# Kernel optimization log

Hardware: AMD Instinct MI355X
Metric: run time of the kernel (lower is better)

Reference implementation:

```python
import jax, jax.numpy as jnp
import numpy as np
import math

EPS = 1e-20
TEMP = 0.07


def _affinity(x1, x2, n):
    # x1, x2: (B, C, T-1, N+1); use only the first n (non-dustbin) nodes
    A = jnp.einsum('bctn,bctm->btnm', x1[..., :n], x2[..., :n])  # (B,T-1,n,n)
    # entropy of row-normalized affinities (intended math of Categorical(probs=A[b,t,k]).entropy())
    p = A / A.sum(-1, keepdims=True)
    ent = -(p * jnp.log(jnp.maximum(p, EPS))).sum(-1)            # (B,T-1,n)
    dustbin_w = 1.0 / math.log(n)
    A = jnp.concatenate([A, (ent * dustbin_w)[..., None]], axis=-1)  # (B,T-1,n,n+1)
    dust_row = -A.sum(-2)[:, :, None, :]                              # (B,T-1,1,n+1)
    A = jnp.concatenate([A, dust_row], axis=2)                        # (B,T-1,n+1,n+1)
    A = A.at[:, :, -1, -1].set(0.0)
    return A


def _l2norm(x, axis):
    return x / jnp.maximum(jnp.linalg.norm(x, axis=axis, keepdims=True), 1e-12)


def _forward(feats_raw, dust_raw, W_self, b_self, W_dust, b_dust):
    B, N, Cenc, T = feats_raw.shape
    # selfsim head: Linear over channel dim, then L2-normalize features
    f = jnp.einsum('bnct,cd->bndt', feats_raw, W_self) + b_self[None, None, :, None]
    f = _l2norm(f, axis=2)                      # (B,N,128,T)
    q = jnp.transpose(f, (0, 2, 3, 1))          # (B,128,T,N)
    d = jnp.einsum('bct,cd->bdt', dust_raw, W_dust) + b_dust[None, :, None]
    d = _l2norm(d, axis=1)                      # (B,128,T)
    q = jnp.concatenate([q, d[..., None]], axis=-1)  # (B,128,T,N+1)

    Af = _affinity(q[:, :, :-1], q[:, :, 1:], N)
    qf = jnp.flip(q, axis=2)
    Ab = _affinity(qf[:, :, :-1], qf[:, :, 1:], N)

    A12 = jax.nn.softmax(Af / TEMP, axis=-1)    # (B,T-1,M,M)
    A21 = jax.nn.softmax(Ab / TEMP, axis=-1)

    M = N + 1
    tgt = jnp.tile(jnp.arange(M), B)            # (B*M,)
    rows = jnp.arange(B * M)
    left = A12[:, 0]
    right = A21[:, T - 2]
    losses = []
    for i in range(1, T - 1):                   # fixed small loop over time steps
        left = left @ A12[:, i]
        right = A21[:, T - 2 - i] @ right
        AA = left @ right                       # (B,M,M) palindrome walk
        logits = jnp.log(AA + EPS).reshape(-1, M)
        ls = jax.nn.log_softmax(logits, axis=-1)
        losses.append(-ls[rows, tgt].mean())
    loss = sum(losses) / len(losses)
    return q, loss


def setup_inputs() -> dict:
    key = jax.random.key(0)
    ks = jax.random.split(key, 4)
    B, N, C, T, D = 4, 784, 512, 8, 128
    return {
        'feats_raw': jax.random.normal(ks[0], (B, N, C, T), dtype=jnp.float32),
        'dust_raw': jax.random.normal(ks[1], (B, C, T), dtype=jnp.float32),
        'W_self': jax.random.normal(ks[2], (C, D), dtype=jnp.float32) * 0.05,
        'b_self': jnp.zeros((D,), dtype=jnp.float32),
        'W_dust': jax.random.normal(ks[3], (C, D), dtype=jnp.float32) * 0.05,
        'b_dust': jnp.zeros((D,), dtype=jnp.float32),
    }


def reference(feats_raw, dust_raw, W_self, b_self, W_dust, b_dust):
    return _forward(feats_raw, dust_raw, W_self, b_self, W_dust, b_dust)
```

## Files before the change

### kernel.cpp

```cpp
#include <hip/hip_runtime.h>
#include <hip/hip_bf16.h>
#include <math.h>

constexpr int Bc = 4;
constexpr int Nc = 784;
constexpr int Cc = 512;
constexpr int Tc = 8;
constexpr int Dc = 128;
constexpr int Mc = 785;
constexpr int TM1 = 7;
constexpr int Pp = 832;
constexpr int Qrows = 896;
constexpr float TEMP = 0.07f;

typedef __attribute__((ext_vector_type(4))) float f32x4;
typedef __attribute__((ext_vector_type(8))) unsigned short u16x8;
typedef __attribute__((ext_vector_type(8))) __bf16 bf16x8;

__device__ __forceinline__ unsigned short f2bf(float v) {
    __hip_bfloat16 h = __float2bfloat16(v);
    return __builtin_bit_cast(unsigned short, h);
}
__device__ __forceinline__ float bf2f(unsigned short u) {
    return __builtin_bit_cast(float, (unsigned int)u << 16);
}

__device__ __forceinline__ void gload16(const void* g, void* l) {
    __builtin_amdgcn_global_load_lds(
        (const __attribute__((address_space(1))) unsigned int*)g,
        (__attribute__((address_space(3))) unsigned int*)l, 16, 0, 0);
}

template<int LD>
__device__ __forceinline__ void mfma_tile_loop(const unsigned short* __restrict__ A,
                                               const unsigned short* __restrict__ BT,
                                               unsigned short* __restrict__ As,
                                               unsigned short* __restrict__ Bs,
                                               int i0, int j0, int tid,
                                               f32x4 (&acc)[4][4])
{
    const int lane = tid & 63, w = tid >> 6;
    const int wr = w >> 1, wc = w & 1;
    const int g = lane >> 4, lr = lane & 15;

    for (int k0 = 0; k0 < LD; k0 += 64) {
        __syncthreads();
        #pragma unroll
        for (int q = 0; q < 4; ++q) {
            int L16 = q * 256 + tid;
            int r = L16 >> 3;
            int csw = ((L16 & 7) << 4) ^ ((r & 7) << 4);
            const char* ga = (const char*)(A  + (size_t)(i0 + r) * LD + k0) + csw;
            const char* gb = (const char*)(BT + (size_t)(j0 + r) * LD + k0) + csw;
            gload16(ga, As + (size_t)L16 * 8);
            gload16(gb, Bs + (size_t)L16 * 8);
        }
        __syncthreads();
        #pragma unroll
        for (int ks = 0; ks < 2; ++ks) {
            bf16x8 af[4], bf[4];
            #pragma unroll
            for (int m = 0; m < 4; ++m) {
                int r = wr * 64 + m * 16 + lr;
                int cb = (ks * 64 + g * 16) ^ ((r & 7) << 4);
                af[m] = __builtin_bit_cast(bf16x8, *(const u16x8*)((const char*)As + r * 128 + cb));
            }
            #pragma unroll
            for (int n = 0; n < 4; ++n) {
                int r = wc * 64 + n * 16 + lr;
                int cb = (ks * 64 + g * 16) ^ ((r & 7) << 4);
                bf[n] = __builtin_bit_cast(bf16x8, *(const u16x8*)((const char*)Bs + r * 128 + cb));
            }
            #pragma unroll
            for (int m = 0; m < 4; ++m)
                #pragma unroll
                for (int n = 0; n < 4; ++n)
                    acc[m][n] = __builtin_amdgcn_mfma_f32_16x16x32_bf16(af[m], bf[n], acc[m][n], 0, 0, 0);
        }
    }
}

__device__ __forceinline__ float blockReduceSum(float v, float* sbuf) {
    #pragma unroll
    for (int off = 32; off; off >>= 1) v += __shfl_down(v, off, 64);
    __syncthreads();
    if ((threadIdx.x & 63) == 0) sbuf[threadIdx.x >> 6] = v;
    __syncthreads();
    return sbuf[0] + sbuf[1] + sbuf[2] + sbuf[3];
}
__device__ __forceinline__ float blockReduceMax(float v, float* sbuf) {
    #pragma unroll
    for (int off = 32; off; off >>= 1) v = fmaxf(v, __shfl_down(v, off, 64));
    __syncthreads();
    if ((threadIdx.x & 63) == 0) sbuf[threadIdx.x >> 6] = v;
    __syncthreads();
    return fmaxf(fmaxf(sbuf[0], sbuf[1]), fmaxf(sbuf[2], sbuf[3]));
}

__global__ __launch_bounds__(256) void k_pack(const float* __restrict__ feats,
                                              unsigned int* __restrict__ Abf32)
{
    __shared__ float lds[Cc * 9];
    int bid = blockIdx.x;
    int b = bid / Nc, n = bid % Nc;
    const float* src = feats + (size_t)(b * Nc + n) * Cc * Tc;
    int tid = threadIdx.x;
    for (int i = tid; i < Cc * Tc; i += 256) lds[(i >> 3) * 9 + (i & 7)] = src[i];
    __syncthreads();
    #pragma unroll
    for (int t = 0; t < Tc; ++t) {
        size_t row = (size_t)(b * Tc + t) * Nc + n;
        float v0 = lds[(2 * tid) * 9 + t];
        float v1 = lds[(2 * tid + 1) * 9 + t];
        unsigned int pk = (unsigned int)f2bf(v0) | ((unsigned int)f2bf(v1) << 16);
        Abf32[row * (Cc / 2) + tid] = pk;
    }
}

__global__ __launch_bounds__(256) void k_packw(const float* __restrict__ Wself,
                                               const float* __restrict__ Wdust,
                                               unsigned short* __restrict__ WTb)
{
    __shared__ float tile[64][65];
    int which = blockIdx.z;
    const float* W = which ? Wdust : Wself;
    unsigned short* O = WTb + (size_t)which * Dc * Cc;
    int d0 = blockIdx.x * 64, c0 = blockIdx.y * 64;
    int tx = threadIdx.x & 63, ty = threadIdx.x >> 6;
    #pragma unroll
    for (int y = 0; y < 64; y += 4) tile[y + ty][tx] = W[(size_t)(c0 + y + ty) * Dc + d0 + tx];
    __syncthreads();
    #pragma unroll
    for (int y = 0; y < 64; y += 4) O[(size_t)(d0 + y + ty) * Cc + c0 + tx] = f2bf(tile[tx][y + ty]);
}

__global__ __launch_bounds__(256, 3) void k_gemm_proj(const unsigned short* __restrict__ A,
                                                      const unsigned short* __restrict__ BT,
                                                      const float* __restrict__ bias,
                                                      float* __restrict__ Cf)
{
    __shared__ __align__(16) unsigned short As[128 * 64];
    __shared__ __align__(16) unsigned short Bs[128 * 64];
    const int i0 = blockIdx.y * 128;
    const int tid = threadIdx.x, lane = tid & 63, w = tid >> 6;
    const int wr = w >> 1, wc = w & 1;
    const int g = lane >> 4, lr = lane & 15;

    f32x4 acc[4][4] = {};
    mfma_tile_loop<Cc>(A, BT, As, Bs, i0, 0, tid, acc);

    #pragma unroll
    for (int n = 0; n < 4; ++n) {
        int col = wc * 64 + n * 16 + lr;
        float bv = bias[col];
        #pragma unroll
        for (int m = 0; m < 4; ++m)
            #pragma unroll
            for (int j = 0; j < 4; ++j) {
                int row = i0 + wr * 64 + m * 16 + g * 4 + j;
                Cf[(size_t)row * Dc + col] = acc[m][n][j] + bv;
            }
    }
}

__global__ __launch_bounds__(128) void k_dustproj(const float* __restrict__ dust,
                                                  const float* __restrict__ Wdust,
                                                  const float* __restrict__ bdust,
                                                  unsigned short* __restrict__ qTb,
                                                  float* __restrict__ qout)
{
    __shared__ float sdust[Cc];
    __shared__ float red[2];
    int bt = blockIdx.x;
    int b = bt >> 3, t = bt & 7;
    int tid = threadIdx.x;
    for (int i = tid; i < Cc; i += 128) sdust[i] = dust[((size_t)b * Cc + i) * Tc + t];
    __syncthreads();
    float acc = 0.f;
    for (int c = 0; c < Cc; ++c) acc += sdust[c] * Wdust[(size_t)c * Dc + tid];
    acc += bdust[tid];
    float s = acc * acc;
    #pragma unroll
    for (int off = 32; off; off >>= 1) s += __shfl_down(s, off, 64);
    if ((tid & 63) == 0) red[tid >> 6] = s;
    __syncthreads();
    float inv = 1.f / fmaxf(sqrtf(red[0] + red[1]), 1e-12f);
    float qv = acc * inv;
    qTb[((size_t)bt * Qrows + Nc) * Dc + tid] = f2bf(qv);
    qout[(((size_t)b * Dc + tid) * Tc + t) * Mc + Nc] = qv;
}

__global__ __launch_bounds__(256) void k_norm(const float* __restrict__ fbuf,
                                              unsigned short* __restrict__ qTb,
                                              float* __restrict__ qout)
{
    __shared__ float lds[64][129];
    __shared__ float nrm[64][4];
    __shared__ float inv[64];
    int bt = blockIdx.y;
    int b = bt >> 3, t = bt & 7;
    int n0 = blockIdx.x * 64;
    int tid = threadIdx.x;
    #pragma unroll
    for (int q = 0; q < 8; ++q) {
        int i = q * 256 + tid;
        int nl = i >> 5, d4 = i & 31;
        f32x4 v = {};
        if (n0 + nl < Nc) v = *(const f32x4*)(fbuf + ((size_t)bt * Nc + n0 + nl) * Dc + d4 * 4);
        *(f32x4*)(&lds[nl][d4 * 4]) = v;
    }
    __syncthreads();
    {
        int r = tid & 63, p = tid >> 6;
        float s = 0.f;
        #pragma unroll
        for (int j = 0; j < 32; ++j) { float v = lds[r][p * 32 + j]; s += v * v; }
        nrm[r][p] = s;
    }
    __syncthreads();
    if (tid < 64) inv[tid] = 1.f / fmaxf(sqrtf(nrm[tid][0] + nrm[tid][1] + nrm[tid][2] + nrm[tid][3]), 1e-12f);
    __syncthreads();
    unsigned int* qT32 = (unsigned int*)(qTb + (size_t)bt * Qrows * Dc);
    #pragma unroll
    for (int q = 0; q < 16; ++q) {
        int i = q * 256 + tid;
        int nl = i >> 6, dp = i & 63;
        if (n0 + nl < Nc) {
            float iv = inv[nl];
            unsigned int pk = (unsigned int)f2bf(lds[nl][2 * dp] * iv)
                            | ((unsigned int)f2bf(lds[nl][2 * dp + 1] * iv) << 16);
            qT32[((size_t)(n0 + nl) * Dc >> 1) + dp] = pk;
        }
    }
    int nl = tid & 63;
    if (n0 + nl < Nc) {
        float iv = inv[nl];
        #pragma unroll
        for (int dd = 0; dd < Dc; dd += 4) {
            int d = dd + (tid >> 6);
            qout[(((size_t)b * Dc + d) * Tc + t) * Mc + n0 + nl] = lds[nl][d] * iv;
        }
    }
}

__global__ __launch_bounds__(256) void k_affinity(const unsigned short* __restrict__ qTb,
                                                  unsigned short* __restrict__ P12h,
                                                  unsigned short* __restrict__ P21h,
                                                  float* __restrict__ cs12,
                                                  float* __restrict__ cs21,
                                                  float wconst)
{
    constexpr float INVT = 1.0f / TEMP;
    const size_t MMp = (size_t)Pp * Pp;
    __shared__ unsigned short otile[16][840];
    __shared__ float sred[16][4][2];
    __shared__ float rowsum[16], invZ[16], entP[16];

    int f = blockIdx.x;
    int xcd = f & 7, slot = f >> 3;
    int grp = xcd + 8 * (slot / 49);
    int strip = slot % 49;
    int side = grp >= 28 ? 1 : 0;
    int bt = grp - side * 28;
    int b = bt / TM1, t = bt % TM1;
    const unsigned short *Aq, *Bq;
    unsigned short* OUT;
    if (side == 0) {
        Aq = qTb + (size_t)(b * Tc + t)     * Qrows * Dc;
        Bq = qTb + (size_t)(b * Tc + t + 1) * Qrows * Dc;
        OUT = P12h + (size_t)bt * MMp;
    } else {
        Aq = qTb + (size_t)(b * Tc + 7 - t) * Qrows * Dc;
        Bq = qTb + (size_t)(b * Tc + 6 - t) * Qrows * Dc;
        OUT = P21h + (size_t)bt * MMp;
    }
    float* csFlip = (side == 0 ? cs21 : cs12) + (size_t)(b * TM1 + (6 - t)) * Pp;

    const int r0 = strip * 16;
    const int tid = threadIdx.x, lane = tid & 63, w = tid >> 6;
    const int g = lane >> 4, lr = lane & 15;

    f32x4 acc[13] = {};
    #pragma unroll
    for (int ks = 0; ks < 4; ++ks) {
        bf16x8 af = __builtin_bit_cast(bf16x8,
            *(const u16x8*)(Aq + (size_t)(r0 + lr) * Dc + ks * 32 + g * 8));
        bf16x8 bfr[7];
        #pragma unroll
        for (int tt = 0; tt < 7; ++tt)
            if (w * 13 + tt < 49)
                bfr[tt] = __builtin_bit_cast(bf16x8,
                    *(const u16x8*)(Bq + (size_t)((w * 13 + tt) * 16 + lr) * Dc + ks * 32 + g * 8));
        #pragma unroll
        for (int tt = 0; tt < 7; ++tt)
            if (w * 13 + tt < 49)
                acc[tt] = __builtin_amdgcn_mfma_f32_16x16x32_bf16(af, bfr[tt], acc[tt], 0, 0, 0);
        #pragma unroll
        for (int tt = 7; tt < 13; ++tt)
            if (w * 13 + tt < 49)
                bfr[tt - 7] = __builtin_bit_cast(bf16x8,
                    *(const u16x8*)(Bq + (size_t)((w * 13 + tt) * 16 + lr) * Dc + ks * 32 + g * 8));
        #pragma unroll
        for (int tt = 7; tt < 13; ++tt)
            if (w * 13 + tt < 49)
                acc[tt] = __builtin_amdgcn_mfma_f32_16x16x32_bf16(af, bfr[tt - 7], acc[tt], 0, 0, 0);
    }

    float rs[4] = {0.f, 0.f, 0.f, 0.f};
    #pragma unroll
    for (int tt = 0; tt < 13; ++tt) {
        if (w * 13 + tt < 49) {
            #pragma unroll
            for (int j = 0; j < 4; ++j) rs[j] += acc[tt][j];
        }
    }
    #pragma unroll
    for (int off = 1; off <= 8; off <<= 1) {
        #pragma unroll
        for (int j = 0; j < 4; ++j) rs[j] += __shfl_xor(rs[j], off, 64);
    }
    if (lr == 0) {
        #pragma unroll
        for (int j = 0; j < 4; ++j) sred[g * 4 + j][w][0] = rs[j];
    }
    __syncthreads();
    if (tid < 16) {
        float r = sred[tid][0][0] + sred[tid][1][0] + sred[tid][2][0] + sred[tid][3][0];
        rowsum[tid] = r;
        csFlip[r0 + tid] = r;
    }
    __syncthreads();

    float invr[4];
    #pragma unroll
    for (int j = 0; j < 4; ++j) invr[j] = 1.0f / rowsum[g * 4 + j];
    float en[4] = {0.f, 0.f, 0.f, 0.f}, es[4] = {0.f, 0.f, 0.f, 0.f};
    #pragma unroll
    for (int tt = 0; tt < 13; ++tt) {
        if (w * 13 + tt < 49) {
            #pragma unroll
            for (int j = 0; j < 4; ++j) {
                float a = acc[tt][j];
                float e = __expf(a * INVT);
                es[j] += e;
                float p = a * invr[j];
                en[j] -= p * __logf(fmaxf(p, 1e-20f));
                acc[tt][j] = e;
            }
        }
    }
    #pragma unroll
    for (int off = 1; off <= 8; off <<= 1) {
        #pragma unroll
        for (int j = 0; j < 4; ++j) {
            es[j] += __shfl_xor(es[j], off, 64);
            en[j] += __shfl_xor(en[j], off, 64);
        }
    }
    if (lr == 0) {
        #pragma unroll
        for (int j = 0; j < 4; ++j) { sred[g * 4 + j][w][0] = es[j]; sred[g * 4 + j][w][1] = en[j]; }
    }
    __syncthreads();
    if (tid < 16) {
        float esum = sred[tid][0][0] + sred[tid][1][0] + sred[tid][2][0] + sred[tid][3][0];
        float ent  = sred[tid][0][1] + sred[tid][1][1] + sred[tid][2][1] + sred[tid][3][1];
        float ez  = __expf(ent * wconst * INVT);
        float Z   = esum + ez;
        float iz  = 1.0f / Z;
        invZ[tid] = iz;
        entP[tid] = ez * iz;
    }
    __syncthreads();

    float izl[4];
    #pragma unroll
    for (int j = 0; j < 4; ++j) izl[j] = invZ[g * 4 + j];
    #pragma unroll
    for (int tt = 0; tt < 13; ++tt) {
        int gt = w * 13 + tt;
        if (gt < 49) {
            int col = gt * 16 + lr;
            #pragma unroll
            for (int j = 0; j < 4; ++j)
                otile[g * 4 + j][col] = f2bf(acc[tt][j] * izl[j]);
        }
    }
    if (tid < 16) otile[tid][784] = f2bf(entP[tid]);
    for (int i = tid; i < 16 * 47; i += 256) otile[i / 47][785 + i % 47] = 0;
    __syncthreads();

    for (int v = tid; v < 16 * 104; v += 256) {
        int row = v / 104, cv = v % 104;
        *(u16x8*)(OUT + (size_t)(r0 + row) * Pp + cv * 8) = *(const u16x8*)(&otile[row][cv * 8]);
    }
}

__global__ __launch_bounds__(256) void k_dustrow(const float* __restrict__ cs12,
                                                 const float* __restrict__ cs21,
                                                 unsigned short* __restrict__ P12h,
                                                 unsigned short* __restrict__ P21h)
{
    constexpr float INVT = 1.0f / TEMP;
    const size_t MMp = (size_t)Pp * Pp;
    int bt = blockIdx.x, side = blockIdx.y;
    const float* cs = (side ? cs21 : cs12) + (size_t)bt * Pp;
    unsigned short* OUT = (side ? P21h : P12h) + (size_t)bt * MMp;
    __shared__ float sbuf[4];
    int tid = threadIdx.x;
    float v[4];
    #pragma unroll
    for (int k = 0; k < 4; ++k) {
        int j = tid + k * 256;
        float val = -INFINITY;
        if (j < Nc)       val = -cs[j] * INVT;
        else if (j == Nc) val = 0.f;
        v[k] = val;
    }
    float mx = fmaxf(fmaxf(v[0], v[1]), fmaxf(v[2], v[3]));
    mx = blockReduceMax(mx, sbuf);
    float e[4]; float s = 0.f;
    #pragma unroll
    for (int k = 0; k < 4; ++k) {
        int j = tid + k * 256;
        e[k] = (j < Mc) ? __expf(v[k] - mx) : 0.f;
        s += e[k];
    }
    s = blockReduceSum(s, sbuf);
    float invs = 1.f / s;
    #pragma unroll
    for (int k = 0; k < 4; ++k) {
        int j = tid + k * 256;
        if (j < Mc)      OUT[(size_t)Nc * Pp + j] = f2bf(e[k] * invs);
        else if (j < Pp) OUT[(size_t)Nc * Pp + j] = 0;
    }
    u16x8 z = {};
    u16x8* dst = (u16x8*)(OUT + (size_t)785 * Pp);
    for (int i = tid; i < (Pp - 785) * Pp / 8; i += 256) dst[i] = z;
}

__global__ __launch_bounds__(256) void k_transpose_bf16(const unsigned short* __restrict__ P12h,
                                                        const unsigned short* __restrict__ P21h,
                                                        unsigned short* __restrict__ Db)
{
    const size_t MMp = (size_t)Pp * Pp;
    __shared__ unsigned short tile[64][65];
    int z = blockIdx.z;
    const unsigned short* S;
    if (z < 24) { int b = z / 6, tm = z % 6; S = P12h + ((size_t)b * 7 + tm + 1) * MMp; }
    else        { S = P21h + ((size_t)(z - 24) * 7 + 6) * MMp; }
    unsigned short* D = Db + (size_t)z * MMp;
    int x0 = blockIdx.x * 64, y0 = blockIdx.y * 64;
    int tx = threadIdx.x & 63, ty = threadIdx.x >> 6;
    #pragma unroll
    for (int y = 0; y < 64; y += 4) tile[y + ty][tx] = S[(size_t)(y0 + y + ty) * Pp + x0 + tx];
    __syncthreads();
    #pragma unroll
    for (int y = 0; y < 64; y += 4) D[(size_t)(x0 + y + ty) * Pp + y0 + tx] = tile[tx][y + ty];
}

struct GJobs {
    const unsigned short* A[2];
    const unsigned short* BT[2];
    unsigned short* Cb[2];
    float* cs[2];
    long long sA[2], sB[2], sC[2];
    const unsigned short* Lr;
    const unsigned short* Rr;
    const float* csL;
    float* loss;
    float scale;
};

__global__ __launch_bounds__(256, 4) void k_gemm_loss(GJobs J)
{
    const size_t MMp = (size_t)Pp * Pp;
    if (blockIdx.x >= 728) {
        int q = blockIdx.x - 728;
        int w = threadIdx.x >> 6, lane = threadIdx.x & 63;
        int r = q * 4 + w;
        int b = r / Mc, i = r % Mc;
        const u16x8* lrow = (const u16x8*)(J.Lr + (size_t)b * MMp + (size_t)i * Pp);
        const u16x8* rrow = (const u16x8*)(J.Rr + (size_t)b * MMp + (size_t)i * Pp);
        const f32x4* cs4  = (const f32x4*)(J.csL + (size_t)b * Pp);
        float sR = 0.f, sD = 0.f;
        for (int c = lane; c < Pp / 8; c += 64) {
            u16x8 lv = lrow[c];
            u16x8 rv = rrow[c];
            f32x4 c0 = cs4[2 * c], c1 = cs4[2 * c + 1];
            #pragma unroll
            for (int k = 0; k < 4; ++k) {
                float fl = bf2f(lv[k]);
                sR += fl * c0[k];
                sD += fl * bf2f(rv[k]);
            }
            #pragma unroll
            for (int k = 0; k < 4; ++k) {
                float fl = bf2f(lv[4 + k]);
                sR += fl * c1[k];
                sD += fl * bf2f(rv[4 + k]);
            }
        }
        #pragma unroll
        for (int off = 1; off <= 32; off <<= 1) {
            sR += __shfl_xor(sR, off, 64);
            sD += __shfl_xor(sD, off, 64);
        }
        if (lane == 0)
            atomicAdd(J.loss, (logf(sR + Mc * 1e-20f) - logf(sD + 1e-20f)) * J.scale);
        return;
    }

    __shared__ __align__(16) unsigned short As[64 * 64];
    __shared__ __align__(16) unsigned short Bs[128 * 64];

    int f = blockIdx.x;
    int zz = f & 7, slot = f >> 3;
    int job = zz >> 2, b = zz & 3;
    const unsigned short* A  = J.A[job]  + (size_t)b * J.sA[job];
    const unsigned short* BT = J.BT[job] + (size_t)b * J.sB[job];

    const int i0 = (slot / 7) * 64, j0 = (slot % 7) * 128;
    const int tid = threadIdx.x, lane = tid & 63, wv = tid >> 6;
    const int g = lane >> 4, lr = lane & 15;

    f32x4 acc[4][2] = {};

    for (int k0 = 0; k0 < Pp; k0 += 64) {
        __syncthreads();
        #pragma unroll
        for (int q = 0; q < 2; ++q) {
            int s = q * 256 + tid;
            int r = s >> 3;
            int csw = ((s & 7) << 4) ^ ((r & 7) << 4);
            gload16((const char*)(A + (size_t)(i0 + r) * Pp + k0) + csw, As + (size_t)s * 8);
        }
        #pragma unroll
        for (int q = 0; q < 4; ++q) {
            int s = q * 256 + tid;
            int r = s >> 3;
            int csw = ((s & 7) << 4) ^ ((r & 7) << 4);
            gload16((const char*)(BT + (size_t)(j0 + r) * Pp + k0) + csw, Bs + (size_t)s * 8);
        }
        __syncthreads();
        #pragma unroll
        for (int ks = 0; ks < 2; ++ks) {
            bf16x8 af[4], bf[2];
            #pragma unroll
            for (int m = 0; m < 4; ++m) {
                int r = m * 16 + lr;
                int cb = (ks * 64 + g * 16) ^ ((r & 7) << 4);
                af[m] = __builtin_bit_cast(bf16x8, *(const u16x8*)((const char*)As + r * 128 + cb));
            }
            #pragma unroll
            for (int n = 0; n < 2; ++n) {
                int r = wv * 32 + n * 16 + lr;
                int cb = (ks * 64 + g * 16) ^ ((r & 7) << 4);
                bf[n] = __builtin_bit_cast(bf16x8, *(const u16x8*)((const char*)Bs + r * 128 + cb));
            }
            #pragma unroll
            for (int m = 0; m < 4; ++m)
                #pragma unroll
                for (int n = 0; n < 2; ++n)
                    acc[m][n] = __builtin_amdgcn_mfma_f32_16x16x32_bf16(af[m], bf[n], acc[m][n], 0, 0, 0);
        }
    }

    unsigned short* Co = J.Cb[job] + (size_t)b * J.sC[job];
    float* csp = J.cs[job];
    float csacc[2] = {0.f, 0.f};
    #pragma unroll
    for (int m = 0; m < 4; ++m)
        #pragma unroll
        for (int n = 0; n < 2; ++n)
            #pragma unroll
            for (int j = 0; j < 4; ++j) {
                int row = i0 + m * 16 + g * 4 + j;
                int col = j0 + wv * 32 + n * 16 + lr;
                if (col < Pp) {
                    unsigned short h = f2bf(acc[m][n][j]);
                    Co[(size_t)row * Pp + col] = h;
                    csacc[n] += bf2f(h);
                }
            }
    if (csp) {
        csp += (size_t)b * Pp;
        #pragma unroll
        for (int n = 0; n < 2; ++n) {
            float p = csacc[n];
            p += __shfl_xor(p, 16, 64);
            p += __shfl_xor(p, 32, 64);
            int col = j0 + wv * 32 + n * 16 + lr;
            if (g == 0 && col < Pp) atomicAdd(&csp[col], p);
        }
    }
}

__global__ __launch_bounds__(64) void k_lossrow(const unsigned short* __restrict__ L,
                                                const unsigned short* __restrict__ R,
                                                const float* __restrict__ csR,
                                                float* __restrict__ loss, float scale)
{
    const size_t MMp = (size_t)Pp * Pp;
    int r = blockIdx.x;
    int b = r / Mc, i = r % Mc;
    const u16x8* lrow = (const u16x8*)(L + (size_t)b * MMp + (size_t)i * Pp);
    const u16x8* rrow = (const u16x8*)(R + (size_t)b * MMp + (size_t)i * Pp);
    const f32x4* cs4  = (const f32x4*)(csR + (size_t)b * Pp);
    int lane = threadIdx.x;
    float sR = 0.f, sD = 0.f;
    for (int c = lane; c < Pp / 8; c += 64) {
        u16x8 lv = lrow[c];
        u16x8 rv = rrow[c];
        f32x4 c0 = cs4[2 * c], c1 = cs4[2 * c + 1];
        #pragma unroll
        for (int k = 0; k < 4; ++k) {
            float fl = bf2f(lv[k]);
            sR += fl * c0[k];
            sD += fl * bf2f(rv[k]);
        }
        #pragma unroll
        for (int k = 0; k < 4; ++k) {
            float fl = bf2f(lv[4 + k]);
            sR += fl * c1[k];
            sD += fl * bf2f(rv[4 + k]);
        }
    }
    #pragma unroll
    for (int off = 1; off <= 32; off <<= 1) {
        sR += __shfl_xor(sR, off, 64);
        sD += __shfl_xor(sD, off, 64);
    }
    if (lane == 0)
        atomicAdd(loss, (logf(sR + Mc * 1e-20f) - logf(sD + 1e-20f)) * scale);
}

extern "C" void kernel_launch(void* const* d_in, const int* in_sizes, int n_in,
                              void* d_out, int out_size, void* d_ws, size_t ws_size,
                              hipStream_t stream)
{
    const float* feats = (const float*)d_in[0];
    const float* dust  = (const float*)d_in[1];
    const float* Wself = (const float*)d_in[2];
    const float* bself = (const float*)d_in[3];
    const float* Wdust = (const float*)d_in[4];
    const float* bdust = (const float*)d_in[5];

    float* out  = (float*)d_out;
    float* qout = out;
    float* loss = out + (size_t)Bc * Dc * Tc * Mc;

    const size_t MMp = (size_t)Pp * Pp;

    float* ws = (float*)d_ws;
    float* csR = ws;
    unsigned short* P12h = (unsigned short*)(ws + 4 * MMp);
    unsigned short* P21h = P12h + (size_t)28 * MMp;
    unsigned short* chainT = P21h + (size_t)28 * MMp;
    unsigned short* P12T  = chainT;
    unsigned short* P21T6 = P12T + (size_t)24 * MMp;
    unsigned short* l0    = P21T6 + (size_t)4 * MMp;
    unsigned short* l1    = l0 + (size_t)4 * MMp;
    unsigned short* R0    = l1 + (size_t)4 * MMp;
    unsigned short* R1    = R0 + (size_t)4 * MMp;
    unsigned short* qTb   = R1 + (size_t)4 * MMp;
    float* cs12 = (float*)(qTb + (size_t)32 * Qrows * Dc);
    float* cs21 = cs12 + (size_t)28 * Pp;

    unsigned short* Abf   = chainT;
    unsigned int*   Abf32 = (unsigned int*)Abf;
    unsigned short* WTb   = Abf + (size_t)Bc * Tc * Nc * Cc;
    float*          fbuf  = (float*)(WTb + 2 * (size_t)Dc * Cc);

    k_pack<<<Bc * Nc, 256, 0, stream>>>(feats, Abf32);
    k_packw<<<dim3(2, 8, 2), 256, 0, stream>>>(Wself, Wdust, WTb);
    hipMemsetAsync(csR, 0, (size_t)6 * Bc * Pp * sizeof(float), stream);
    hipMemsetAsync(loss, 0, sizeof(float), stream);
    k_gemm_proj<<<dim3(1, 196), 256, 0, stream>>>(Abf, WTb, bself, fbuf);
    k_dustproj<<<32, 128, 0, stream>>>(dust, Wdust, bdust, qTb, qout);
    k_norm<<<dim3(13, 32), 256, 0, stream>>>(fbuf, qTb, qout);
    float wconst = (float)(1.0 / log(784.0));
    k_affinity<<<2744, 256, 0, stream>>>(qTb, P12h, P21h, cs12, cs21, wconst);
    k_dustrow<<<dim3(28, 2), 256, 0, stream>>>(cs12, cs21, P12h, P21h);
    k_transpose_bf16<<<dim3(13, 13, 28), 256, 0, stream>>>(P12h, P21h, P12T);

    const float scale = 1.0f / (6.0f * Bc * Mc);

    {
        GJobs J = {};
        J.A[0] = P12h;  J.sA[0] = (long long)7 * MMp;
        J.BT[0] = P12T; J.sB[0] = (long long)6 * MMp;
        J.Cb[0] = l0;   J.sC[0] = (long long)MMp; J.cs[0] = nullptr;
        J.A[1] = P21T6;                   J.sA[1] = (long long)MMp;
        J.BT[1] = P21h + (size_t)5 * MMp; J.sB[1] = (long long)7 * MMp;
        J.Cb[1] = R0;   J.sC[1] = (long long)MMp; J.cs[1] = csR;
        k_gemm_loss<<<728, 256, 0, stream>>>(J);
    }

    unsigned short *lcur = l0, *lnxt = l1, *rcur = R0, *rnxt = R1;
    for (int i = 1; i <= 5; ++i) {
        GJobs J = {};
        J.A[0] = lcur; J.sA[0] = (long long)MMp;
        J.BT[0] = P12T + (size_t)i * MMp; J.sB[0] = (long long)6 * MMp;
        J.Cb[0] = lnxt; J.sC[0] = (long long)MMp; J.cs[0] = nullptr;
        J.A[1] = rcur; J.sA[1] = (long long)MMp;
        J.BT[1] = P21h + (size_t)(5 - i) * MMp; J.sB[1] = (long long)7 * MMp;
        J.Cb[1] = rnxt; J.sC[1] = (long long)MMp; J.cs[1] = csR + (size_t)i * Bc * Pp;
        J.Lr = lcur; J.Rr = rcur; J.csL = csR + (size_t)(i - 1) * Bc * Pp;
        J.loss = loss; J.scale = scale;
        k_gemm_loss<<<728 + 785, 256, 0, stream>>>(J);
        unsigned short* t;
        t = lcur; lcur = lnxt; lnxt = t;
        t = rcur; rcur = rnxt; rnxt = t;
    }
    k_lossrow<<<Bc * Mc, 64, 0, stream>>>(lcur, rcur, csR + (size_t)5 * Bc * Pp, loss, scale);
}
```

Measured before the change: 481.6 us.

## Double-buffer GEMM tiles, shrink projection tiles, and fuse small setup kernels

Adds a shared double-buffered 64x128 MFMA GEMM helper that prefetches the next K-tile into a second LDS buffer while the current one is computed, and uses it in both the projection GEMM and the loss-chain GEMM. The projection GEMM moves from 128x128 tiles on 196 blocks to 64x128 tiles on 392 blocks. Weight packing, buffer zeroing and the dustbin projection are folded into existing kernels as extra blocks, which removes separate launches and memsets. Launch bounds are changed (affinity 2 waves/SIMD hint, loss GEMM from 4 to 3) to fit the doubled LDS, at the cost of lower occupancy.

```diff
diff --git a/kernel.cpp b/kernel.cpp
--- a/kernel.cpp
+++ b/kernel.cpp
@@ -32,51 +32,74 @@
 }
 
 template<int LD>
-__device__ __forceinline__ void mfma_tile_loop(const unsigned short* __restrict__ A,
-                                               const unsigned short* __restrict__ BT,
-                                               unsigned short* __restrict__ As,
-                                               unsigned short* __restrict__ Bs,
-                                               int i0, int j0, int tid,
-                                               f32x4 (&acc)[4][4])
-{
-    const int lane = tid & 63, w = tid >> 6;
-    const int wr = w >> 1, wc = w & 1;
+__device__ __forceinline__ void gemm64x128_db(const unsigned short* __restrict__ A,
+                                              const unsigned short* __restrict__ BT,
+                                              unsigned short* As0, unsigned short* As1,
+                                              unsigned short* Bs0, unsigned short* Bs1,
+                                              int i0, int j0, int tid, f32x4 (&acc)[4][2])
+{
+    const int lane = tid & 63, wv = tid >> 6;
     const int g = lane >> 4, lr = lane & 15;
-
-    for (int k0 = 0; k0 < LD; k0 += 64) {
-        __syncthreads();
-        #pragma unroll
-        for (int q = 0; q < 4; ++q) {
-            int L16 = q * 256 + tid;
-            int r = L16 >> 3;
-            int csw = ((L16 & 7) << 4) ^ ((r & 7) << 4);
-            const char* ga = (const char*)(A  + (size_t)(i0 + r) * LD + k0) + csw;
-            const char* gb = (const char*)(BT + (size_t)(j0 + r) * LD + k0) + csw;
-            gload16(ga, As + (size_t)L16 * 8);
-            gload16(gb, Bs + (size_t)L16 * 8);
-        }
-        __syncthreads();
+    constexpr int NT = LD / 64;
+
+    #pragma unroll
+    for (int q = 0; q < 2; ++q) {
+        int s = q * 256 + tid; int r = s >> 3;
+        int csw = ((s & 7) << 4) ^ ((r & 7) << 4);
+        gload16((const char*)(A + (size_t)(i0 + r) * LD) + csw, As0 + (size_t)s * 8);
+    }
+    #pragma unroll
+    for (int q = 0; q < 4; ++q) {
+        int s = q * 256 + tid; int r = s >> 3;
+        int csw = ((s & 7) << 4) ^ ((r & 7) << 4);
+        gload16((const char*)(BT + (size_t)(j0 + r) * LD) + csw, Bs0 + (size_t)s * 8);
+    }
+    __syncthreads();
+
+    for (int t = 0; t < NT; ++t) {
+        unsigned short* Asc = (t & 1) ? As1 : As0;
+        unsigned short* Bsc = (t & 1) ? Bs1 : Bs0;
+        if (t + 1 < NT) {
+            int k0 = (t + 1) * 64;
+            unsigned short* Asn = (t & 1) ? As0 : As1;
+            unsigned short* Bsn = (t & 1) ? Bs0 : Bs1;
+            #pragma unroll
+            for (int q = 0; q < 2; ++q) {
+                int s = q * 256 + tid; int r = s >> 3;
+                int csw = ((s & 7) << 4) ^ ((r & 7) << 4);
+                gload16((const char*)(A + (size_t)(i0 + r) * LD + k0) + csw, Asn + (size_t)s * 8);
+            }
+            #pragma unroll
+            for (int q = 0; q < 4; ++q) {
+                int s = q * 256 + tid; int r = s >> 3;
+                int csw = ((s & 7) << 4) ^ ((r & 7) << 4);
+                gload16((const char*)(BT + (size_t)(j0 + r) * LD + k0) + csw, Bsn + (size_t)s * 8);
+            }
+        }
+        bf16x8 af[2][4], bf[2][2];
         #pragma unroll
         for (int ks = 0; ks < 2; ++ks) {
-            bf16x8 af[4], bf[4];
             #pragma unroll
             for (int m = 0; m < 4; ++m) {
-                int r = wr * 64 + m * 16 + lr;
+                int r = m * 16 + lr;
                 int cb = (ks * 64 + g * 16) ^ ((r & 7) << 4);
-                af[m] = __builtin_bit_cast(bf16x8, *(const u16x8*)((const char*)As + r * 128 + cb));
-            }
-            #pragma unroll
-            for (int n = 0; n < 4; ++n) {
-                int r = wc * 64 + n * 16 + lr;
+                af[ks][m] = __builtin_bit_cast(bf16x8, *(const u16x8*)((const char*)Asc + r * 128 + cb));
+            }
+            #pragma unroll
+            for (int n = 0; n < 2; ++n) {
+                int r = wv * 32 + n * 16 + lr;
                 int cb = (ks * 64 + g * 16) ^ ((r & 7) << 4);
-                bf[n] = __builtin_bit_cast(bf16x8, *(const u16x8*)((const char*)Bs + r * 128 + cb));
-            }
+                bf[ks][n] = __builtin_bit_cast(bf16x8, *(const u16x8*)((const char*)Bsc + r * 128 + cb));
+            }
+        }
+        #pragma unroll
+        for (int ks = 0; ks < 2; ++ks)
             #pragma unroll
             for (int m = 0; m < 4; ++m)
                 #pragma unroll
-                for (int n = 0; n < 4; ++n)
-                    acc[m][n] = __builtin_amdgcn_mfma_f32_16x16x32_bf16(af[m], bf[n], acc[m][n], 0, 0, 0);
-        }
+                for (int n = 0; n < 2; ++n)
+                    acc[m][n] = __builtin_amdgcn_mfma_f32_16x16x32_bf16(af[ks][m], bf[ks][n], acc[m][n], 0, 0, 0);
+        __syncthreads();
     }
 }
 
@@ -98,13 +121,39 @@
 }
 
 __global__ __launch_bounds__(256) void k_pack(const float* __restrict__ feats,
-                                              unsigned int* __restrict__ Abf32)
+                                              const float* __restrict__ Wself,
+                                              const float* __restrict__ Wdust,
+                                              unsigned int* __restrict__ Abf32,
+                                              unsigned short* __restrict__ WTb,
+                                              float* __restrict__ csR,
+                                              float* __restrict__ loss)
 {
     __shared__ float lds[Cc * 9];
     int bid = blockIdx.x;
+    int tid = threadIdx.x;
+    if (bid == Bc * Nc + 32) {
+        int n = 6 * Bc * Pp;
+        for (int i = tid; i < n; i += 256) csR[i] = 0.f;
+        if (tid == 0) *loss = 0.f;
+        return;
+    }
+    if (bid >= Bc * Nc) {
+        int pidx = bid - Bc * Nc;
+        int which = pidx >> 4;
+        int rem = pidx & 15;
+        int d0 = (rem >> 3) * 64, c0 = (rem & 7) * 64;
+        const float* W = which ? Wdust : Wself;
+        unsigned short* O = WTb + (size_t)which * Dc * Cc;
+        int tx = tid & 63, ty = tid >> 6;
+        #pragma unroll
+        for (int y = 0; y < 64; y += 4) lds[(y + ty) * 65 + tx] = W[(size_t)(c0 + y + ty) * Dc + d0 + tx];
+        __syncthreads();
+        #pragma unroll
+        for (int y = 0; y < 64; y += 4) O[(size_t)(d0 + y + ty) * Cc + c0 + tx] = f2bf(lds[tx * 65 + y + ty]);
+        return;
+    }
     int b = bid / Nc, n = bid % Nc;
     const float* src = feats + (size_t)(b * Nc + n) * Cc * Tc;
-    int tid = threadIdx.x;
     for (int i = tid; i < Cc * Tc; i += 256) lds[(i >> 3) * 9 + (i & 7)] = src[i];
     __syncthreads();
     #pragma unroll
@@ -117,90 +166,73 @@
     }
 }
 
-__global__ __launch_bounds__(256) void k_packw(const float* __restrict__ Wself,
-                                               const float* __restrict__ Wdust,
-                                               unsigned short* __restrict__ WTb)
-{
-    __shared__ float tile[64][65];
-    int which = blockIdx.z;
-    const float* W = which ? Wdust : Wself;
-    unsigned short* O = WTb + (size_t)which * Dc * Cc;
-    int d0 = blockIdx.x * 64, c0 = blockIdx.y * 64;
-    int tx = threadIdx.x & 63, ty = threadIdx.x >> 6;
-    #pragma unroll
-    for (int y = 0; y < 64; y += 4) tile[y + ty][tx] = W[(size_t)(c0 + y + ty) * Dc + d0 + tx];
-    __syncthreads();
-    #pragma unroll
-    for (int y = 0; y < 64; y += 4) O[(size_t)(d0 + y + ty) * Cc + c0 + tx] = f2bf(tile[tx][y + ty]);
-}
-
 __global__ __launch_bounds__(256, 3) void k_gemm_proj(const unsigned short* __restrict__ A,
                                                       const unsigned short* __restrict__ BT,
                                                       const float* __restrict__ bias,
                                                       float* __restrict__ Cf)
 {
-    __shared__ __align__(16) unsigned short As[128 * 64];
-    __shared__ __align__(16) unsigned short Bs[128 * 64];
-    const int i0 = blockIdx.y * 128;
-    const int tid = threadIdx.x, lane = tid & 63, w = tid >> 6;
-    const int wr = w >> 1, wc = w & 1;
+    __shared__ __align__(16) unsigned short As0[64 * 64], As1[64 * 64];
+    __shared__ __align__(16) unsigned short Bs0[128 * 64], Bs1[128 * 64];
+    const int i0 = blockIdx.x * 64;
+    const int tid = threadIdx.x, lane = tid & 63, wv = tid >> 6;
     const int g = lane >> 4, lr = lane & 15;
 
-    f32x4 acc[4][4] = {};
-    mfma_tile_loop<Cc>(A, BT, As, Bs, i0, 0, tid, acc);
-
-    #pragma unroll
-    for (int n = 0; n < 4; ++n) {
-        int col = wc * 64 + n * 16 + lr;
+    f32x4 acc[4][2] = {};
+    gemm64x128_db<Cc>(A, BT, As0, As1, Bs0, Bs1, i0, 0, tid, acc);
+
+    #pragma unroll
+    for (int n = 0; n < 2; ++n) {
+        int col = wv * 32 + n * 16 + lr;
         float bv = bias[col];
         #pragma unroll
         for (int m = 0; m < 4; ++m)
             #pragma unroll
             for (int j = 0; j < 4; ++j) {
-                int row = i0 + wr * 64 + m * 16 + g * 4 + j;
+                int row = i0 + m * 16 + g * 4 + j;
                 Cf[(size_t)row * Dc + col] = acc[m][n][j] + bv;
             }
     }
 }
 
-__global__ __launch_bounds__(128) void k_dustproj(const float* __restrict__ dust,
-                                                  const float* __restrict__ Wdust,
-                                                  const float* __restrict__ bdust,
-                                                  unsigned short* __restrict__ qTb,
-                                                  float* __restrict__ qout)
-{
-    __shared__ float sdust[Cc];
-    __shared__ float red[2];
-    int bt = blockIdx.x;
-    int b = bt >> 3, t = bt & 7;
-    int tid = threadIdx.x;
-    for (int i = tid; i < Cc; i += 128) sdust[i] = dust[((size_t)b * Cc + i) * Tc + t];
-    __syncthreads();
-    float acc = 0.f;
-    for (int c = 0; c < Cc; ++c) acc += sdust[c] * Wdust[(size_t)c * Dc + tid];
-    acc += bdust[tid];
-    float s = acc * acc;
-    #pragma unroll
-    for (int off = 32; off; off >>= 1) s += __shfl_down(s, off, 64);
-    if ((tid & 63) == 0) red[tid >> 6] = s;
-    __syncthreads();
-    float inv = 1.f / fmaxf(sqrtf(red[0] + red[1]), 1e-12f);
-    float qv = acc * inv;
-    qTb[((size_t)bt * Qrows + Nc) * Dc + tid] = f2bf(qv);
-    qout[(((size_t)b * Dc + tid) * Tc + t) * Mc + Nc] = qv;
-}
-
 __global__ __launch_bounds__(256) void k_norm(const float* __restrict__ fbuf,
+                                              const float* __restrict__ dust,
+                                              const float* __restrict__ Wdust,
+                                              const float* __restrict__ bdust,
                                               unsigned short* __restrict__ qTb,
                                               float* __restrict__ qout)
 {
     __shared__ float lds[64][129];
     __shared__ float nrm[64][4];
     __shared__ float inv[64];
+    __shared__ float red2[2];
     int bt = blockIdx.y;
     int b = bt >> 3, t = bt & 7;
+    int tid = threadIdx.x;
+
+    if (blockIdx.x == 13) {
+        float* sdust = &lds[0][0];
+        for (int i = tid; i < Cc; i += 256) sdust[i] = dust[((size_t)b * Cc + i) * Tc + t];
+        __syncthreads();
+        float acc = 0.f;
+        if (tid < 128) {
+            for (int c = 0; c < Cc; ++c) acc += sdust[c] * Wdust[(size_t)c * Dc + tid];
+            acc += bdust[tid];
+            float s = acc * acc;
+            #pragma unroll
+            for (int off = 32; off; off >>= 1) s += __shfl_down(s, off, 64);
+            if ((tid & 63) == 0) red2[tid >> 6] = s;
+        }
+        __syncthreads();
+        if (tid < 128) {
+            float inv0 = 1.f / fmaxf(sqrtf(red2[0] + red2[1]), 1e-12f);
+            float qv = acc * inv0;
+            qTb[((size_t)bt * Qrows + Nc) * Dc + tid] = f2bf(qv);
+            qout[(((size_t)b * Dc + tid) * Tc + t) * Mc + Nc] = qv;
+        }
+        return;
+    }
+
     int n0 = blockIdx.x * 64;
-    int tid = threadIdx.x;
     #pragma unroll
     for (int q = 0; q < 8; ++q) {
         int i = q * 256 + tid;
@@ -243,12 +275,12 @@
     }
 }
 
-__global__ __launch_bounds__(256) void k_affinity(const unsigned short* __restrict__ qTb,
-                                                  unsigned short* __restrict__ P12h,
-                                                  unsigned short* __restrict__ P21h,
-                                                  float* __restrict__ cs12,
-                                                  float* __restrict__ cs21,
-                                                  float wconst)
+__global__ __launch_bounds__(256, 2) void k_affinity(const unsigned short* __restrict__ qTb,
+                                                     unsigned short* __restrict__ P12h,
+                                                     unsigned short* __restrict__ P21h,
+                                                     float* __restrict__ cs12,
+                                                     float* __restrict__ cs21,
+                                                     float wconst)
 {
     constexpr float INVT = 1.0f / TEMP;
     const size_t MMp = (size_t)Pp * Pp;
@@ -472,7 +504,7 @@
     float scale;
 };
 
-__global__ __launch_bounds__(256, 4) void k_gemm_loss(GJobs J)
+__global__ __launch_bounds__(256, 3) void k_gemm_loss(GJobs J)
 {
     const size_t MMp = (size_t)Pp * Pp;
     if (blockIdx.x >= 728) {
@@ -511,8 +543,8 @@
         return;
     }
 
-    __shared__ __align__(16) unsigned short As[64 * 64];
-    __shared__ __align__(16) unsigned short Bs[128 * 64];
+    __shared__ __align__(16) unsigned short As0[64 * 64], As1[64 * 64];
+    __shared__ __align__(16) unsigned short Bs0[128 * 64], Bs1[128 * 64];
 
     int f = blockIdx.x;
     int zz = f & 7, slot = f >> 3;
@@ -525,46 +557,7 @@
     const int g = lane >> 4, lr = lane & 15;
 
     f32x4 acc[4][2] = {};
-
-    for (int k0 = 0; k0 < Pp; k0 += 64) {
-        __syncthreads();
-        #pragma unroll
-        for (int q = 0; q < 2; ++q) {
-            int s = q * 256 + tid;
-            int r = s >> 3;
-            int csw = ((s & 7) << 4) ^ ((r & 7) << 4);
-            gload16((const char*)(A + (size_t)(i0 + r) * Pp + k0) + csw, As + (size_t)s * 8);
-        }
-        #pragma unroll
-        for (int q = 0; q < 4; ++q) {
-            int s = q * 256 + tid;
-            int r = s >> 3;
-            int csw = ((s & 7) << 4) ^ ((r & 7) << 4);
-            gload16((const char*)(BT + (size_t)(j0 + r) * Pp + k0) + csw, Bs + (size_t)s * 8);
-        }
-        __syncthreads();
-        #pragma unroll
-        for (int ks = 0; ks < 2; ++ks) {
-            bf16x8 af[4], bf[2];
-            #pragma unroll
-            for (int m = 0; m < 4; ++m) {
-                int r = m * 16 + lr;
-                int cb = (ks * 64 + g * 16) ^ ((r & 7) << 4);
-                af[m] = __builtin_bit_cast(bf16x8, *(const u16x8*)((const char*)As + r * 128 + cb));
-            }
-            #pragma unroll
-            for (int n = 0; n < 2; ++n) {
-                int r = wv * 32 + n * 16 + lr;
-                int cb = (ks * 64 + g * 16) ^ ((r & 7) << 4);
-                bf[n] = __builtin_bit_cast(bf16x8, *(const u16x8*)((const char*)Bs + r * 128 + cb));
-            }
-            #pragma unroll
-            for (int m = 0; m < 4; ++m)
-                #pragma unroll
-                for (int n = 0; n < 2; ++n)
-                    acc[m][n] = __builtin_amdgcn_mfma_f32_16x16x32_bf16(af[m], bf[n], acc[m][n], 0, 0, 0);
-        }
-    }
+    gemm64x128_db<Pp>(A, BT, As0, As1, Bs0, Bs1, i0, j0, tid, acc);
 
     unsigned short* Co = J.Cb[job] + (size_t)b * J.sC[job];
     float* csp = J.cs[job];
@@ -672,13 +665,9 @@
     unsigned short* WTb   = Abf + (size_t)Bc * Tc * Nc * Cc;
     float*          fbuf  = (float*)(WTb + 2 * (size_t)Dc * Cc);
 
-    k_pack<<<Bc * Nc, 256, 0, stream>>>(feats, Abf32);
-    k_packw<<<dim3(2, 8, 2), 256, 0, stream>>>(Wself, Wdust, WTb);
-    hipMemsetAsync(csR, 0, (size_t)6 * Bc * Pp * sizeof(float), stream);
-    hipMemsetAsync(loss, 0, sizeof(float), stream);
-    k_gemm_proj<<<dim3(1, 196), 256, 0, stream>>>(Abf, WTb, bself, fbuf);
-    k_dustproj<<<32, 128, 0, stream>>>(dust, Wdust, bdust, qTb, qout);
-    k_norm<<<dim3(13, 32), 256, 0, stream>>>(fbuf, qTb, qout);
+    k_pack<<<Bc * Nc + 32 + 1, 256, 0, stream>>>(feats, Wself, Wdust, Abf32, WTb, csR, loss);
+    k_gemm_proj<<<392, 256, 0, stream>>>(Abf, WTb, bself, fbuf);
+    k_norm<<<dim3(14, 32), 256, 0, stream>>>(fbuf, dust, Wdust, bdust, qTb, qout);
     float wconst = (float)(1.0 / log(784.0));
     k_affinity<<<2744, 256, 0, stream>>>(qTb, P12h, P21h, cs12, cs21, wconst);
     k_dustrow<<<dim3(28, 2), 256, 0, stream>>>(cs12, cs21, P12h, P21h);
```

Measured after the change: 445.5 us. -7.5%, faster.
